# Performance work log

Measured on AMD Instinct MI355X. Metric: run time of the kernel, lower is better.

## Reference

```python
import jax, jax.numpy as jnp
import numpy as np

NUM_HEADS = 8


def setup_inputs() -> dict:
    key = jax.random.key(0)
    ks = jax.random.split(key, 8)
    B, N, H, W = 8, 1024, 32, 32
    dim = H * W  # 1024
    x1 = jax.random.normal(ks[0], (B, N, H, W), dtype=jnp.float32)
    x2 = jax.random.normal(ks[1], (B, N, H, W), dtype=jnp.float32)
    conv_w = jax.random.normal(ks[2], (N, 2 * N, 3, 3), dtype=jnp.float32) * 0.01
    conv_b = jnp.zeros((N,), dtype=jnp.float32)
    wq = jax.random.normal(ks[3], (dim, dim), dtype=jnp.float32) * 0.02
    wk = jax.random.normal(ks[4], (dim, dim), dtype=jnp.float32) * 0.02
    wv = jax.random.normal(ks[5], (dim, dim), dtype=jnp.float32) * 0.02
    proj_w = jax.random.normal(ks[6], (dim, dim), dtype=jnp.float32) * 0.02
    proj_b = jnp.zeros((dim,), dtype=jnp.float32)
    return {"x1": x1, "x2": x2, "conv_w": conv_w, "conv_b": conv_b,
            "wq": wq, "wk": wk, "wv": wv, "proj_w": proj_w, "proj_b": proj_b}


def reference(x1, x2, conv_w, conv_b, wq, wk, wv, proj_w, proj_b):
    B, N, H, W = x1.shape
    C = H * W
    nh = NUM_HEADS
    hd = C // nh
    scale = hd ** -0.5

    # conv_cat: Conv2d(2N -> N, k=3, pad=1) on channel-concatenated inputs
    x_cat = jnp.concatenate([x1, x2], axis=1)  # [B, 2N, H, W]
    x_cat = jax.lax.conv_general_dilated(
        x_cat, conv_w, window_strides=(1, 1), padding=((1, 1), (1, 1)),
        dimension_numbers=("NCHW", "OIHW", "NCHW"))
    x_cat = x_cat + conv_b[None, :, None, None]
    x_cat = x_cat.reshape(B, N, C)  # [B, N, C]

    # torch Linear: y = x @ W.T (no bias, qkv_bias=False)
    def heads(t):  # [B, N, C] -> [B, nh, N, hd]
        return t.reshape(B, N, nh, hd).transpose(0, 2, 1, 3)

    q = heads(x1.reshape(B, N, C) @ wq.T)
    k = heads(x_cat @ wk.T)
    v = heads(x_cat @ wv.T)

    # attention: softmax(q k^T * scale) v   (dropout is identity at p=0)
    attn = jnp.einsum("bhnd,bhmd->bhnm", q, k) * scale
    attn = jax.nn.softmax(attn, axis=-1)
    x_attn = jnp.einsum("bhnm,bhmd->bhnd", attn, v)  # [B, nh, N, hd]
    x_attn = x_attn.transpose(0, 2, 1, 3).reshape(B, N, C)

    out = (x_attn @ proj_w.T + proj_b).reshape(B, N, H, W) + x1
    return out
```

## Files before the change

### kernel.cpp

```cpp
#include <hip/hip_runtime.h>
#include <hip/hip_bf16.h>
#include <cstdint>
#include <cstddef>

typedef __attribute__((ext_vector_type(8))) short short8;
typedef __attribute__((ext_vector_type(4))) float f32x4;
typedef unsigned short u16;

static __device__ __forceinline__ u16 f2bf(float f) {
  __hip_bfloat16 h = __float2bfloat16(f);
  return *reinterpret_cast<u16*>(&h);
}

static __device__ __forceinline__ void gload16(const void* g, void* l) {
  __builtin_amdgcn_global_load_lds(
      (const __attribute__((address_space(1))) void*)g,
      (__attribute__((address_space(3))) void*)l, 16, 0, 0);
}


__global__ void cast4_k(const float* __restrict__ a, const float* __restrict__ b,
                        const float* __restrict__ c, const float* __restrict__ d,
                        u16* __restrict__ oa, u16* __restrict__ ob,
                        u16* __restrict__ oc, u16* __restrict__ od) {
  const int which = blockIdx.y;
  const float* src = (which == 0) ? a : (which == 1) ? b : (which == 2) ? c : d;
  u16* dst = (which == 0) ? oa : (which == 1) ? ob : (which == 2) ? oc : od;
  int i = blockIdx.x * 256 + threadIdx.x;
  float4 v = ((const float4*)src)[i];
  union { u16 u[4]; uint2 p; } r;
  r.u[0] = f2bf(v.x); r.u[1] = f2bf(v.y); r.u[2] = f2bf(v.z); r.u[3] = f2bf(v.w);
  ((uint2*)dst)[i] = r.p;
}

__global__ void build_int2(const float* __restrict__ x1, const float* __restrict__ x2,
                           u16* __restrict__ in_t, u16* __restrict__ x1b) {
  __shared__ float tile[64][65];
  const int it = blockIdx.x;
  const int st = blockIdx.y;
  const int b  = blockIdx.z;
  const int i0 = it * 64, s0 = st * 64;
  const bool isx1 = (i0 < 1024);
  const float* src = isx1
      ? x1 + ((size_t)b * 1024 + i0) * 1024
      : x2 + ((size_t)b * 1024 + (i0 - 1024)) * 1024;
  const int t = threadIdx.x;
  #pragma unroll
  for (int jj = 0; jj < 16; ++jj) {
    int idx = jj * 256 + t;
    int ii = idx >> 6, si = idx & 63;
    float v = src[(size_t)ii * 1024 + s0 + si];
    tile[ii][si] = v;
    if (isx1)
      x1b[((size_t)b * 1024 + i0 + ii) * 1024 + s0 + si] = f2bf(v);
  }
  __syncthreads();
  #pragma unroll
  for (int jj = 0; jj < 16; ++jj) {
    int idx = jj * 256 + t;
    int si = idx >> 6, ii = idx & 63;
    in_t[((size_t)b * 1024 + s0 + si) * 2048 + i0 + ii] = f2bf(tile[ii][si]);
  }
}

__global__ void pack_wp(const float* __restrict__ cw, u16* __restrict__ Wp) {
  __shared__ float sb[2304];
  const int blk = blockIdx.x;
  const int t = threadIdx.x;
  const size_t base = (size_t)blk * 2304;
  #pragma unroll
  for (int jj = 0; jj < 9; ++jj) sb[jj * 256 + t] = cw[base + jj * 256 + t];
  __syncthreads();
  const int p = blk * 256 + t;
  #pragma unroll
  for (int q = 0; q < 9; ++q)
    Wp[(size_t)q * 2097152 + p] = f2bf(sb[t * 9 + q]);
}

__global__ void zero_k(u16* z) { z[threadIdx.x] = 0; }

__global__ void addc_k(const float* __restrict__ p, const float* __restrict__ bias,
                       u16* __restrict__ xc) {
  __shared__ float tile[64][65];
  const int st = blockIdx.x;
  const int ot = blockIdx.y;
  const int b  = blockIdx.z;
  const int s0 = st * 64, o0 = ot * 64;
  const int t = threadIdx.x;
  const float* p1 = p + 8388608;
  #pragma unroll
  for (int jj = 0; jj < 16; ++jj) {
    int idx = jj * 256 + t;
    int si = idx >> 6, oi = idx & 63;
    const size_t m = ((size_t)b * 1024 + s0 + si) * 1024 + o0 + oi;
    tile[si][oi] = p[m] + p1[m] + bias[o0 + oi];
  }
  __syncthreads();
  #pragma unroll
  for (int jj = 0; jj < 16; ++jj) {
    int idx = jj * 256 + t;
    int oi = idx >> 6, si = idx & 63;
    xc[((size_t)b * 1024 + o0 + oi) * 1024 + s0 + si] = f2bf(tile[si][oi]);
  }
}

enum { GM_PLAIN = 0, GM_VT = 1, GM_PROJ = 2, GM_CONV = 3, GM_KV = 4 };

template<int MODE>
__global__ __launch_bounds__(512, 2)
void gemm3_k(const u16* __restrict__ A, const u16* __restrict__ B,
             u16* __restrict__ Cb, float* __restrict__ Cf,
             const float* __restrict__ bias, const float* __restrict__ resid,
             int Ktot, int ntn_sh) {
  __shared__ u16 lds[3 * 24576];
  const int tid = threadIdx.x;
  const int lane = tid & 63;
  const int w = tid >> 6;
  const int l15 = lane & 15, l4 = lane >> 4;

  const int nwg = gridDim.x;
  const int bid = blockIdx.x;
  const int lb = (bid & 7) * (nwg >> 3) + (bid >> 3);
  const int tm = lb >> ntn_sh;
  const int tn = lb & ((1 << ntn_sh) - 1);
  const int row0 = tm * 256, col0 = tn * 128;
  const int wr = (w >> 1) * 64, wc = (w & 1) * 64;

  const int sr = w * 8 + (lane >> 3);
  const int pp = (lane & 7) ^ (lane >> 3);

  f32x4 acc[4][4];
  #pragma unroll
  for (int i = 0; i < 4; ++i)
    #pragma unroll
    for (int jj = 0; jj < 4; ++jj)
      acc[i][jj] = (f32x4){0.f, 0.f, 0.f, 0.f};

  const int nK = Ktot >> 6;

  auto stage = [&](int kt, u16* buf) {
    u16* da = buf + (size_t)w * 512;
    u16* db = buf + 16384 + (size_t)w * 512;
    const int k0 = kt << 6;
    #pragma unroll
    for (int u = 0; u < 4; ++u) {
      const u16* ga = A + (size_t)(row0 + u * 64 + sr) * Ktot + k0 + pp * 8;
      gload16(ga, da + u * 4096);
    }
    #pragma unroll
    for (int u = 0; u < 2; ++u) {
      const u16* gb = B + (size_t)(col0 + u * 64 + sr) * Ktot + k0 + pp * 8;
      gload16(gb, db + u * 4096);
    }
  };

  auto compute = [&](const u16* buf) {
    const char* Ar = (const char*)buf;
    const char* Br = (const char*)(buf + 16384);
    #pragma unroll
    for (int ks = 0; ks < 2; ++ks) {
      const int bcol = ((ks << 6) + (l4 << 4)) ^ ((l15 & 7) << 4);
      short8 av[4], bv[4];
      #pragma unroll
      for (int mi = 0; mi < 4; ++mi)
        av[mi] = *(const short8*)(Ar + (wr + mi * 16 + l15) * 128 + bcol);
      #pragma unroll
      for (int ni = 0; ni < 4; ++ni)
        bv[ni] = *(const short8*)(Br + (wc + ni * 16 + l15) * 128 + bcol);
      __builtin_amdgcn_s_setprio(1);
      #pragma unroll
      for (int mi = 0; mi < 4; ++mi)
        #pragma unroll
        for (int ni = 0; ni < 4; ++ni)
          acc[mi][ni] = __builtin_amdgcn_mfma_f32_16x16x32_bf16(av[mi], bv[ni], acc[mi][ni], 0, 0, 0);
      __builtin_amdgcn_s_setprio(0);
    }
  };

  u16* pb0 = lds;
  u16* pb1 = lds + 24576;
  u16* pb2 = lds + 49152;

  stage(0, pb0);
  stage(1, pb1);
  for (int t = 0; t < nK; ++t) {
    if (t + 1 < nK) {
      asm volatile("s_waitcnt vmcnt(6)" ::: "memory");
    } else {
      asm volatile("s_waitcnt vmcnt(0)" ::: "memory");
    }
    __builtin_amdgcn_s_barrier();
    if (t + 2 < nK) stage(t + 2, pb2);
    compute(pb0);
    u16* tmp = pb0; pb0 = pb1; pb1 = pb2; pb2 = tmp;
  }

  #pragma unroll
  for (int mi = 0; mi < 4; ++mi) {
    #pragma unroll
    for (int ni = 0; ni < 4; ++ni) {
      #pragma unroll
      for (int j = 0; j < 4; ++j) {
        const int grow = row0 + wr + mi * 16 + l4 * 4 + j;
        const int gcol = col0 + wc + ni * 16 + l15;
        const float v = acc[mi][ni][j];
        if constexpr (MODE == GM_PLAIN) {
          Cb[((size_t)grow << 10) + gcol] = f2bf(v);
        } else if constexpr (MODE == GM_PROJ) {
          const size_t o = ((size_t)grow << 10) + gcol;
          Cf[o] = v + bias[gcol] + resid[o];
        }
      }
    }
  }
}

template<int MODE>
__global__ __launch_bounds__(512, 4)
void gemm5_k(const u16* __restrict__ A, const u16* __restrict__ B,
             u16* __restrict__ Cb, u16* __restrict__ Cb2,
             const u16* __restrict__ zb, int Ktot, int ntn_sh) {
  __shared__ u16 lds[3 * 12288];
  const int tid = threadIdx.x;
  const int lane = tid & 63;
  const int w = tid >> 6;
  const int l15 = lane & 15, l4 = lane >> 4;

  const int nwg = gridDim.x;
  const int bid = blockIdx.x;
  const int lb = (bid & 7) * (nwg >> 3) + (bid >> 3);
  const int tm = lb >> ntn_sh;
  const int tn = lb & ((1 << ntn_sh) - 1);
  const int row0 = tm * 256, col0 = tn * 128;
  const int wr = (w >> 1) * 64, wc = (w & 1) * 64;

  const int str = tid >> 2;
  const int sgc = tid & 3;

  f32x4 acc[4][4];
  #pragma unroll
  for (int i = 0; i < 4; ++i)
    #pragma unroll
    for (int jj = 0; jj < 4; ++jj)
      acc[i][jj] = (f32x4){0.f, 0.f, 0.f, 0.f};

  const int nKt = Ktot >> 5;

  auto stage = [&](int kt, u16* buf) {
    const int k0 = kt << 5;
    #pragma unroll
    for (int u = 0; u < 2; ++u) {
      const int r = u * 128 + str;
      const int swz = sgc ^ ((r >> 1) & 3);
      const u16* ga = A + (size_t)(row0 + r) * Ktot + k0 + swz * 8;
      gload16(ga, buf + ((size_t)u * 512 + tid) * 8);
    }
    {
      const int swz = sgc ^ ((str >> 1) & 3);
      const u16* gb = B + (size_t)(col0 + str) * Ktot + k0 + swz * 8;
      gload16(gb, buf + 8192 + (size_t)tid * 8);
    }
  };

  auto compute = [&](const u16* buf) {
    short8 av[4], bv[4];
    #pragma unroll
    for (int mi = 0; mi < 4; ++mi) {
      const int row = wr + mi * 16 + l15;
      const int g = l4 ^ ((row >> 1) & 3);
      av[mi] = *(const short8*)(buf + row * 32 + g * 8);
    }
    #pragma unroll
    for (int ni = 0; ni < 4; ++ni) {
      const int row = wc + ni * 16 + l15;
      const int g = l4 ^ ((row >> 1) & 3);
      bv[ni] = *(const short8*)(buf + 8192 + row * 32 + g * 8);
    }
    __builtin_amdgcn_s_setprio(1);
    #pragma unroll
    for (int mi = 0; mi < 4; ++mi)
      #pragma unroll
      for (int ni = 0; ni < 4; ++ni)
        acc[mi][ni] = __builtin_amdgcn_mfma_f32_16x16x32_bf16(av[mi], bv[ni], acc[mi][ni], 0, 0, 0);
    __builtin_amdgcn_s_setprio(0);
  };

  u16* pb0 = lds;
  u16* pb1 = lds + 12288;
  u16* pb2 = lds + 24576;

  stage(0, pb0);
  stage(1, pb1);
  for (int t = 0; t < nKt; ++t) {
    if (t + 1 < nKt) {
      asm volatile("s_waitcnt vmcnt(3)" ::: "memory");
    } else {
      asm volatile("s_waitcnt vmcnt(0)" ::: "memory");
    }
    __builtin_amdgcn_s_barrier();
    if (t + 2 < nKt) stage(t + 2, pb2);
    compute(pb0);
    u16* tmp = pb0; pb0 = pb1; pb1 = pb2; pb2 = tmp;
  }

  #pragma unroll
  for (int mi = 0; mi < 4; ++mi) {
    #pragma unroll
    for (int ni = 0; ni < 4; ++ni) {
      #pragma unroll
      for (int j = 0; j < 4; ++j) {
        const int grow = row0 + wr + mi * 16 + l4 * 4 + j;
        const int gcol = col0 + wc + ni * 16 + l15;
        const float v = acc[mi][ni][j];
        if constexpr (MODE == GM_KV) {
          if (gcol < 1024) {
            Cb[((size_t)grow << 10) + gcol] = f2bf(v);
          } else {
            const int c = gcol - 1024;
            const int b = grow >> 10, ms = grow & 1023;
            const int h = c >> 7, d = c & 127;
            Cb2[((size_t)((b * 8 + h) * 128 + d) << 10) + ms] = f2bf(v);
          }
        }
      }
    }
  }
}

template<int SPLITK>
__global__ __launch_bounds__(256, 2)
void gemm6_k(const u16* __restrict__ A, const u16* __restrict__ B,
             float* __restrict__ Cf, const u16* __restrict__ zb,
             int Ktot, int ntn_sh) {
  __shared__ u16 lds[3 * 12288];
  const int tid = threadIdx.x;
  const int lane = tid & 63;
  const int w = tid >> 6;
  const int l15 = lane & 15, l4 = lane >> 4;

  const int nwg = gridDim.x;
  const int bid = blockIdx.x;
  const int lb = (bid & 7) * (nwg >> 3) + (bid >> 3);
  int kz = 0, lbt = lb;
  if constexpr (SPLITK) { kz = lb >> 8; lbt = lb & 255; }
  const int tm = lbt >> ntn_sh;
  const int tn = lbt & ((1 << ntn_sh) - 1);
  const int row0 = tm * 256, col0 = tn * 128;
  const int wr = w * 64;

  const int str = tid >> 2;
  const int sgc = tid & 3;
  const int swz = sgc ^ ((str >> 1) & 3);

  int am[4], ay[4], ax[4];
  #pragma unroll
  for (int u = 0; u < 4; ++u) {
    const int m = row0 + u * 64 + str;
    am[u] = m;
    const int s = m & 1023;
    ay[u] = s >> 5; ax[u] = s & 31;
  }

  f32x4 acc[4][8];
  #pragma unroll
  for (int i = 0; i < 4; ++i)
    #pragma unroll
    for (int jj = 0; jj < 8; ++jj)
      acc[i][jj] = (f32x4){0.f, 0.f, 0.f, 0.f};

  const int nKt = Ktot >> 5;
  const int kbase = SPLITK ? kz * Ktot : 0;

  auto stage = [&](int kt, u16* buf) {
    const int gk0 = kbase + (kt << 5);
    const int q = gk0 >> 11;
    const int ks0 = gk0 & 2047;
    const int qd = (q >= 6) ? 2 : (q >= 3) ? 1 : 0;
    const int dy = qd - 1, dx = q - qd * 3 - 1;
    const int dd = (dy << 5) + dx;
    #pragma unroll
    for (int u = 0; u < 4; ++u) {
      const int yy = ay[u] + dy, xx = ax[u] + dx;
      const bool valid = ((unsigned)yy < 32u) && ((unsigned)xx < 32u);
      const u16* ga = valid ? A + (((size_t)(am[u] + dd)) << 11) + ks0 + swz * 8 : zb;
      gload16(ga, buf + ((size_t)u * 256 + tid) * 8);
    }
    #pragma unroll
    for (int u = 0; u < 2; ++u) {
      const u16* gb = B + ((size_t)q << 21) + ((size_t)(col0 + u * 64 + str) << 11) + ks0 + swz * 8;
      gload16(gb, buf + 8192 + ((size_t)u * 256 + tid) * 8);
    }
  };

  auto compute = [&](const u16* buf) {
    short8 av[4], bv[8];
    #pragma unroll
    for (int mi = 0; mi < 4; ++mi) {
      const int row = wr + mi * 16 + l15;
      const int g = l4 ^ ((row >> 1) & 3);
      av[mi] = *(const short8*)(buf + row * 32 + g * 8);
    }
    #pragma unroll
    for (int ni = 0; ni < 8; ++ni) {
      const int row = ni * 16 + l15;
      const int g = l4 ^ ((row >> 1) & 3);
      bv[ni] = *(const short8*)(buf + 8192 + row * 32 + g * 8);
    }
    __builtin_amdgcn_s_setprio(1);
    #pragma unroll
    for (int mi = 0; mi < 4; ++mi)
      #pragma unroll
      for (int ni = 0; ni < 8; ++ni)
        acc[mi][ni] = __builtin_amdgcn_mfma_f32_16x16x32_bf16(av[mi], bv[ni], acc[mi][ni], 0, 0, 0);
    __builtin_amdgcn_s_setprio(0);
  };

  u16* pb0 = lds;
  u16* pb1 = lds + 12288;
  u16* pb2 = lds + 24576;

  stage(0, pb0);
  stage(1, pb1);
  for (int t = 0; t < nKt; ++t) {
    if (t + 1 < nKt) {
      asm volatile("s_waitcnt vmcnt(6)" ::: "memory");
    } else {
      asm volatile("s_waitcnt vmcnt(0)" ::: "memory");
    }
    __builtin_amdgcn_s_barrier();
    if (t + 2 < nKt) stage(t + 2, pb2);
    compute(pb0);
    u16* tmp = pb0; pb0 = pb1; pb1 = pb2; pb2 = tmp;
  }

  #pragma unroll
  for (int mi = 0; mi < 4; ++mi) {
    #pragma unroll
    for (int ni = 0; ni < 8; ++ni) {
      #pragma unroll
      for (int j = 0; j < 4; ++j) {
        const int grow = row0 + wr + mi * 16 + l4 * 4 + j;
        const int gcol = col0 + ni * 16 + l15;
        Cf[(size_t)kz * 8388608 + ((size_t)grow << 10) + gcol] = acc[mi][ni][j];
      }
    }
  }
}

__global__ __launch_bounds__(256, 2)
void attn2_k(const u16* __restrict__ Q, const u16* __restrict__ K,
             const u16* __restrict__ Vt, u16* __restrict__ O) {
  __shared__ u16 Ks[2][64 * 128];
  __shared__ u16 Vs[2][128 * 64];
  __shared__ u16 Plds[4][16 * 80];
  const int mtile = blockIdx.x;
  const int bh = blockIdx.y;
  const int b = bh >> 3, h = bh & 7;
  const int tid = threadIdx.x, lane = tid & 63, w = tid >> 6;
  const int l15 = lane & 15, l4 = lane >> 4;

  short8 qf[4];
  {
    const int qrow = b * 1024 + mtile * 64 + w * 16 + l15;
    const u16* qb = Q + ((size_t)qrow << 10) + h * 128;
    #pragma unroll
    for (int kk = 0; kk < 4; ++kk)
      qf[kk] = *(const short8*)(qb + kk * 32 + l4 * 8);
  }

  f32x4 o[8];
  #pragma unroll
  for (int db = 0; db < 8; ++db) o[db] = (f32x4){0.f, 0.f, 0.f, 0.f};
  float mrow[4], lrow[4];
  #pragma unroll
  for (int j = 0; j < 4; ++j) { mrow[j] = -1e30f; lrow[j] = 0.f; }
  const float scale = 0.08838834764831845f;

  auto stageKV = [&](int kt, int half) {
    #pragma unroll
    for (int j = 0; j < 4; ++j) {
      const int c = (j * 4 + w) * 64 + lane;
      const int r = c >> 4;
      const int coff = (((c & 15) ^ (r & 7)) << 3);
      const u16* gp = K + ((size_t)(b * 1024 + kt * 64 + r) << 10) + h * 128 + coff;
      gload16(gp, (void*)(Ks[half] + (j * 4 + w) * 512));
    }
    #pragma unroll
    for (int j = 0; j < 4; ++j) {
      const int c = (j * 4 + w) * 64 + lane;
      const int r = c >> 3;
      const int coff = (((c & 7) ^ (r & 7)) << 3);
      const u16* gp = Vt + ((size_t)((b * 8 + h) * 128 + r) << 10) + kt * 64 + coff;
      gload16(gp, (void*)(Vs[half] + (j * 4 + w) * 512));
    }
  };

  stageKV(0, 0);
  for (int kt = 0; kt < 16; ++kt) {
    const int cur = kt & 1;
    asm volatile("s_waitcnt vmcnt(0)" ::: "memory");
    __builtin_amdgcn_s_barrier();
    if (kt + 1 < 16) stageKV(kt + 1, cur ^ 1);

    const u16* ks_ = Ks[cur];
    const u16* vs_ = Vs[cur];
    f32x4 s[4];
    #pragma unroll
    for (int cb = 0; cb < 4; ++cb) {
      s[cb] = (f32x4){0.f, 0.f, 0.f, 0.f};
      #pragma unroll
      for (int kk = 0; kk < 4; ++kk) {
        const int col = (kk * 32 + l4 * 8) ^ ((l15 & 7) << 3);
        short8 bK = *(const short8*)(ks_ + (cb * 16 + l15) * 128 + col);
        s[cb] = __builtin_amdgcn_mfma_f32_16x16x32_bf16(qf[kk], bK, s[cb], 0, 0, 0);
      }
    }
    #pragma unroll
    for (int cb = 0; cb < 4; ++cb) {
      s[cb][0] *= scale; s[cb][1] *= scale; s[cb][2] *= scale; s[cb][3] *= scale;
    }
    #pragma unroll
    for (int j = 0; j < 4; ++j) {
      float mx = fmaxf(fmaxf(s[0][j], s[1][j]), fmaxf(s[2][j], s[3][j]));
      #pragma unroll
      for (int off = 8; off >= 1; off >>= 1)
        mx = fmaxf(mx, __shfl_xor(mx, off, 64));
      const float mn = fmaxf(mrow[j], mx);
      const float fac = __expf(mrow[j] - mn);
      mrow[j] = mn;
      float rs = 0.f;
      #pragma unroll
      for (int cb = 0; cb < 4; ++cb) {
        const float p = __expf(s[cb][j] - mn);
        s[cb][j] = p;
        rs += p;
      }
      #pragma unroll
      for (int off = 8; off >= 1; off >>= 1)
        rs += __shfl_xor(rs, off, 64);
      lrow[j] = lrow[j] * fac + rs;
      #pragma unroll
      for (int db = 0; db < 8; ++db) o[db][j] *= fac;
    }
    u16* pl = Plds[w];
    #pragma unroll
    for (int cb = 0; cb < 4; ++cb)
      #pragma unroll
      for (int j = 0; j < 4; ++j)
        pl[(l4 * 4 + j) * 80 + cb * 16 + l15] = f2bf(s[cb][j]);
    asm volatile("s_waitcnt lgkmcnt(0)" ::: "memory");
    __builtin_amdgcn_sched_barrier(0);
    short8 ap[2];
    #pragma unroll
    for (int ks2 = 0; ks2 < 2; ++ks2)
      ap[ks2] = *(const short8*)(pl + l15 * 80 + ks2 * 32 + l4 * 8);
    #pragma unroll
    for (int db = 0; db < 8; ++db) {
      #pragma unroll
      for (int ks2 = 0; ks2 < 2; ++ks2) {
        const int col = (ks2 * 32 + l4 * 8) ^ ((l15 & 7) << 3);
        short8 bV = *(const short8*)(vs_ + (db * 16 + l15) * 64 + col);
        o[db] = __builtin_amdgcn_mfma_f32_16x16x32_bf16(ap[ks2], bV, o[db], 0, 0, 0);
      }
    }
  }
  #pragma unroll
  for (int db = 0; db < 8; ++db) {
    #pragma unroll
    for (int j = 0; j < 4; ++j) {
      const int grow = b * 1024 + mtile * 64 + w * 16 + l4 * 4 + j;
      const int gcol = h * 128 + db * 16 + l15;
      O[((size_t)grow << 10) + gcol] = f2bf(o[db][j] / lrow[j]);
    }
  }
}


extern "C" void kernel_launch(void* const* d_in, const int* in_sizes, int n_in,
                              void* d_out, int out_size, void* d_ws, size_t ws_size,
                              hipStream_t stream) {
  const float* x1     = (const float*)d_in[0];
  const float* x2     = (const float*)d_in[1];
  const float* conv_w = (const float*)d_in[2];
  const float* conv_b = (const float*)d_in[3];
  const float* wq     = (const float*)d_in[4];
  const float* wk     = (const float*)d_in[5];
  const float* wv     = (const float*)d_in[6];
  const float* proj_w = (const float*)d_in[7];
  const float* proj_b = (const float*)d_in[8];
  float* out = (float*)d_out;

  char* ws = (char*)d_ws;
  size_t off = 0;
  auto alloc = [&](size_t bytes) -> void* {
    void* p = ws + off;
    off += (bytes + 255) & ~(size_t)255;
    return p;
  };
  u16* x1b  = (u16*)alloc(8192ULL * 1024 * 2);
  u16* in_t = (u16*)alloc(8ULL * 1024 * 2048 * 2);
  u16* Wp   = (u16*)alloc(9ULL * 2097152 * 2);
  u16* wqb  = (u16*)alloc(1048576ULL * 2);
  u16* wkb  = (u16*)alloc(1048576ULL * 2);
  u16* wvb  = (u16*)alloc(1048576ULL * 2);
  u16* pjb  = (u16*)alloc(1048576ULL * 2);
  u16* xc   = (u16*)alloc(8192ULL * 1024 * 2);
  u16* Qb   = (u16*)alloc(8192ULL * 1024 * 2);
  u16* Kb   = (u16*)alloc(8192ULL * 1024 * 2);
  u16* Vtb  = (u16*)alloc(8192ULL * 1024 * 2);
  u16* Ob   = (u16*)alloc(8192ULL * 1024 * 2);
  u16* zb   = (u16*)alloc(256);
  float* pConv = (float*)Qb;

  cast4_k<<<dim3(1024, 4), 256, 0, stream>>>(wq, wk, wv, proj_w, wqb, wkb, wvb, pjb);
  build_int2<<<dim3(32, 16, 8), 256, 0, stream>>>(x1, x2, in_t, x1b);
  pack_wp<<<8192, 256, 0, stream>>>(conv_w, Wp);
  zero_k<<<1, 128, 0, stream>>>(zb);

  gemm6_k<1><<<512, 256, 0, stream>>>(in_t, Wp, pConv, zb, 9216, 3);
  addc_k<<<dim3(16, 16, 8), 256, 0, stream>>>(pConv, conv_b, xc);
  gemm3_k<GM_PLAIN><<<256, 512, 0, stream>>>(x1b, wqb, Qb, nullptr, nullptr, nullptr, 1024, 3);
  gemm5_k<GM_KV><<<512, 512, 0, stream>>>(xc, wkb, Kb, Vtb, zb, 1024, 4);
  attn2_k<<<dim3(16, 64), 256, 0, stream>>>(Qb, Kb, Vtb, Ob);
  gemm3_k<GM_PROJ><<<256, 512, 0, stream>>>(Ob, pjb, nullptr, out, proj_b, x1, 1024, 3);
}
```

Baseline: 573.7 us.

## Replace implicit-GEMM conv with padded-halo conv kernel reusing staged input across taps

The input transpose now writes into a zero-padded 34x34 spatial layout, cleared first with a memset, so the conv needs no bounds checks or zero-buffer redirects. A new conv kernel stages a halo tile of input rows (8 image rows plus borders) per 32-channel chunk once, and reuses it across all nine filter taps by offsetting LDS row indices, streaming only the per-tap weight tiles. This cuts repeated global loads of the shifted input, 9x per channel chunk in the old version, at the cost of a memset over the padded buffer and more complex vmcnt/barrier scheduling.

```diff
diff --git a/kernel.cpp b/kernel.cpp
--- a/kernel.cpp
+++ b/kernel.cpp
@@ -33,8 +33,8 @@
   ((uint2*)dst)[i] = r.p;
 }
 
-__global__ void build_int2(const float* __restrict__ x1, const float* __restrict__ x2,
-                           u16* __restrict__ in_t, u16* __restrict__ x1b) {
+__global__ void build_pad(const float* __restrict__ x1, const float* __restrict__ x2,
+                          u16* __restrict__ in_t_pad, u16* __restrict__ x1b) {
   __shared__ float tile[64][65];
   const int it = blockIdx.x;
   const int st = blockIdx.y;
@@ -59,7 +59,9 @@
   for (int jj = 0; jj < 16; ++jj) {
     int idx = jj * 256 + t;
     int si = idx >> 6, ii = idx & 63;
-    in_t[((size_t)b * 1024 + s0 + si) * 2048 + i0 + ii] = f2bf(tile[ii][si]);
+    const int s = s0 + si;
+    const int prow = (b * 34 + (s >> 5) + 1) * 34 + (s & 31) + 1;
+    in_t_pad[(size_t)prow * 2048 + i0 + ii] = f2bf(tile[ii][si]);
   }
 }
 
@@ -76,8 +78,6 @@
   for (int q = 0; q < 9; ++q)
     Wp[(size_t)q * 2097152 + p] = f2bf(sb[t * 9 + q]);
 }
-
-__global__ void zero_k(u16* z) { z[threadIdx.x] = 0; }
 
 __global__ void addc_k(const float* __restrict__ p, const float* __restrict__ bias,
                        u16* __restrict__ xc) {
@@ -104,7 +104,139 @@
   }
 }
 
-enum { GM_PLAIN = 0, GM_VT = 1, GM_PROJ = 2, GM_CONV = 3, GM_KV = 4 };
+enum { GM_PLAIN = 0, GM_PROJ = 2, GM_KV = 4 };
+
+__global__ __launch_bounds__(256, 2)
+void conv7_k(const u16* __restrict__ Ap, const u16* __restrict__ B,
+             float* __restrict__ Cf) {
+  __shared__ u16 lds[2 * 12288 + 3 * 4096];
+  const int tid = threadIdx.x;
+  const int lane = tid & 63, w = tid >> 6;
+  const int l15 = lane & 15, l4 = lane >> 4;
+
+  const int bid = blockIdx.x;
+  const int lb = (bid & 7) * 64 + (bid >> 3);
+  const int kz = lb >> 8;
+  const int tile = lb & 255;
+  const int tm = tile >> 3, tn = tile & 7;
+  const int row0 = tm * 256, col0 = tn * 128;
+  const int b = tm >> 2;
+  const int y0 = (tm & 3) * 8;
+  const int hb = (b * 34 + y0) * 34;
+  const int wr = w * 64;
+  const int chbase = kz * 1024;
+
+  int pr[4];
+  #pragma unroll
+  for (int mi = 0; mi < 4; ++mi) {
+    const int m = row0 + wr + mi * 16 + l15;
+    const int y = (m >> 5) & 31, x = m & 31;
+    pr[mi] = (y - y0 + 1) * 34 + x + 1;
+  }
+
+  const int srow = tid >> 2;
+  const int sgc = tid & 3;
+
+  f32x4 acc[4][8];
+  #pragma unroll
+  for (int i = 0; i < 4; ++i)
+    #pragma unroll
+    for (int jj = 0; jj < 8; ++jj)
+      acc[i][jj] = (f32x4){0.f, 0.f, 0.f, 0.f};
+
+  auto stageHalo = [&](int cc, int half) {
+    u16* dst = lds + half * 12288;
+    #pragma unroll
+    for (int rnd = 0; rnd < 6; ++rnd) {
+      const int row = rnd * 64 + srow;
+      const int g = sgc ^ ((row >> 1) & 3);
+      const u16* src = Ap + (size_t)(hb + row) * 2048 + chbase + cc * 32 + g * 8;
+      gload16(src, dst + (size_t)(rnd * 256 + tid) * 8);
+    }
+  };
+  auto stageB = [&](int cc, int q) {
+    u16* dst = lds + 24576 + (q % 3) * 4096;
+    #pragma unroll
+    for (int rnd = 0; rnd < 2; ++rnd) {
+      const int r = rnd * 64 + srow;
+      const int g = sgc ^ ((r >> 1) & 3);
+      const u16* src = B + ((size_t)q << 21) + (size_t)(col0 + r) * 2048
+                       + chbase + cc * 32 + g * 8;
+      gload16(src, dst + (size_t)(rnd * 256 + tid) * 8);
+    }
+  };
+
+  constexpr int ddt[9] = {-35, -34, -33, -1, 0, 1, 33, 34, 35};
+  constexpr int NC = 32;
+
+  stageHalo(0, 0);
+  stageHalo(1, 1);
+  stageB(0, 0);
+  stageB(0, 1);
+
+  for (int cc = 0; cc < NC; ++cc) {
+    const u16* hcur = lds + (cc & 1) * 12288;
+    const bool interior = (cc >= 1 && cc <= NC - 2);
+    #pragma unroll
+    for (int q = 0; q < 9; ++q) {
+      if ((q == 1 || q == 2) && interior) {
+        asm volatile("s_waitcnt vmcnt(8)" ::: "memory");
+      } else if (q == 8 && cc == NC - 1) {
+        asm volatile("s_waitcnt vmcnt(0)" ::: "memory");
+      } else {
+        asm volatile("s_waitcnt vmcnt(2)" ::: "memory");
+      }
+      __builtin_amdgcn_s_barrier();
+      {
+        const int gp2 = cc * 9 + q + 2;
+        if (gp2 <= NC * 9 - 1) {
+          int qS = q + 2, ccS = cc;
+          if (qS >= 9) { qS -= 9; ccS += 1; }
+          stageB(ccS, qS);
+        }
+        if (q == 0 && cc >= 1 && cc <= NC - 2)
+          stageHalo(cc + 1, (cc + 1) & 1);
+      }
+      {
+        const u16* bq = lds + 24576 + (q % 3) * 4096;
+        const int dd = ddt[q];
+        short8 av[4], bv[8];
+        #pragma unroll
+        for (int mi = 0; mi < 4; ++mi) {
+          const int hr = pr[mi] + dd;
+          const int g = l4 ^ ((hr >> 1) & 3);
+          av[mi] = *(const short8*)(hcur + hr * 32 + g * 8);
+        }
+        #pragma unroll
+        for (int ni = 0; ni < 8; ++ni) {
+          const int r = ni * 16 + l15;
+          const int g = l4 ^ ((r >> 1) & 3);
+          bv[ni] = *(const short8*)(bq + r * 32 + g * 8);
+        }
+        __builtin_amdgcn_s_setprio(1);
+        #pragma unroll
+        for (int mi = 0; mi < 4; ++mi)
+          #pragma unroll
+          for (int ni = 0; ni < 8; ++ni)
+            acc[mi][ni] = __builtin_amdgcn_mfma_f32_16x16x32_bf16(av[mi], bv[ni], acc[mi][ni], 0, 0, 0);
+        __builtin_amdgcn_s_setprio(0);
+      }
+    }
+  }
+
+  #pragma unroll
+  for (int mi = 0; mi < 4; ++mi) {
+    #pragma unroll
+    for (int ni = 0; ni < 8; ++ni) {
+      #pragma unroll
+      for (int j = 0; j < 4; ++j) {
+        const int grow = row0 + wr + mi * 16 + l4 * 4 + j;
+        const int gcol = col0 + ni * 16 + l15;
+        Cf[(size_t)kz * 8388608 + ((size_t)grow << 10) + gcol] = acc[mi][ni][j];
+      }
+    }
+  }
+}
 
 template<int MODE>
 __global__ __launch_bounds__(512, 2)
@@ -219,7 +351,7 @@
 __global__ __launch_bounds__(512, 4)
 void gemm5_k(const u16* __restrict__ A, const u16* __restrict__ B,
              u16* __restrict__ Cb, u16* __restrict__ Cb2,
-             const u16* __restrict__ zb, int Ktot, int ntn_sh) {
+             int Ktot, int ntn_sh) {
   __shared__ u16 lds[3 * 12288];
   const int tid = threadIdx.x;
   const int lane = tid & 63;
@@ -327,126 +459,6 @@
   }
 }
 
-template<int SPLITK>
-__global__ __launch_bounds__(256, 2)
-void gemm6_k(const u16* __restrict__ A, const u16* __restrict__ B,
-             float* __restrict__ Cf, const u16* __restrict__ zb,
-             int Ktot, int ntn_sh) {
-  __shared__ u16 lds[3 * 12288];
-  const int tid = threadIdx.x;
-  const int lane = tid & 63;
-  const int w = tid >> 6;
-  const int l15 = lane & 15, l4 = lane >> 4;
-
-  const int nwg = gridDim.x;
-  const int bid = blockIdx.x;
-  const int lb = (bid & 7) * (nwg >> 3) + (bid >> 3);
-  int kz = 0, lbt = lb;
-  if constexpr (SPLITK) { kz = lb >> 8; lbt = lb & 255; }
-  const int tm = lbt >> ntn_sh;
-  const int tn = lbt & ((1 << ntn_sh) - 1);
-  const int row0 = tm * 256, col0 = tn * 128;
-  const int wr = w * 64;
-
-  const int str = tid >> 2;
-  const int sgc = tid & 3;
-  const int swz = sgc ^ ((str >> 1) & 3);
-
-  int am[4], ay[4], ax[4];
-  #pragma unroll
-  for (int u = 0; u < 4; ++u) {
-    const int m = row0 + u * 64 + str;
-    am[u] = m;
-    const int s = m & 1023;
-    ay[u] = s >> 5; ax[u] = s & 31;
-  }
-
-  f32x4 acc[4][8];
-  #pragma unroll
-  for (int i = 0; i < 4; ++i)
-    #pragma unroll
-    for (int jj = 0; jj < 8; ++jj)
-      acc[i][jj] = (f32x4){0.f, 0.f, 0.f, 0.f};
-
-  const int nKt = Ktot >> 5;
-  const int kbase = SPLITK ? kz * Ktot : 0;
-
-  auto stage = [&](int kt, u16* buf) {
-    const int gk0 = kbase + (kt << 5);
-    const int q = gk0 >> 11;
-    const int ks0 = gk0 & 2047;
-    const int qd = (q >= 6) ? 2 : (q >= 3) ? 1 : 0;
-    const int dy = qd - 1, dx = q - qd * 3 - 1;
-    const int dd = (dy << 5) + dx;
-    #pragma unroll
-    for (int u = 0; u < 4; ++u) {
-      const int yy = ay[u] + dy, xx = ax[u] + dx;
-      const bool valid = ((unsigned)yy < 32u) && ((unsigned)xx < 32u);
-      const u16* ga = valid ? A + (((size_t)(am[u] + dd)) << 11) + ks0 + swz * 8 : zb;
-      gload16(ga, buf + ((size_t)u * 256 + tid) * 8);
-    }
-    #pragma unroll
-    for (int u = 0; u < 2; ++u) {
-      const u16* gb = B + ((size_t)q << 21) + ((size_t)(col0 + u * 64 + str) << 11) + ks0 + swz * 8;
-      gload16(gb, buf + 8192 + ((size_t)u * 256 + tid) * 8);
-    }
-  };
-
-  auto compute = [&](const u16* buf) {
-    short8 av[4], bv[8];
-    #pragma unroll
-    for (int mi = 0; mi < 4; ++mi) {
-      const int row = wr + mi * 16 + l15;
-      const int g = l4 ^ ((row >> 1) & 3);
-      av[mi] = *(const short8*)(buf + row * 32 + g * 8);
-    }
-    #pragma unroll
-    for (int ni = 0; ni < 8; ++ni) {
-      const int row = ni * 16 + l15;
-      const int g = l4 ^ ((row >> 1) & 3);
-      bv[ni] = *(const short8*)(buf + 8192 + row * 32 + g * 8);
-    }
-    __builtin_amdgcn_s_setprio(1);
-    #pragma unroll
-    for (int mi = 0; mi < 4; ++mi)
-      #pragma unroll
-      for (int ni = 0; ni < 8; ++ni)
-        acc[mi][ni] = __builtin_amdgcn_mfma_f32_16x16x32_bf16(av[mi], bv[ni], acc[mi][ni], 0, 0, 0);
-    __builtin_amdgcn_s_setprio(0);
-  };
-
-  u16* pb0 = lds;
-  u16* pb1 = lds + 12288;
-  u16* pb2 = lds + 24576;
-
-  stage(0, pb0);
-  stage(1, pb1);
-  for (int t = 0; t < nKt; ++t) {
-    if (t + 1 < nKt) {
-      asm volatile("s_waitcnt vmcnt(6)" ::: "memory");
-    } else {
-      asm volatile("s_waitcnt vmcnt(0)" ::: "memory");
-    }
-    __builtin_amdgcn_s_barrier();
-    if (t + 2 < nKt) stage(t + 2, pb2);
-    compute(pb0);
-    u16* tmp = pb0; pb0 = pb1; pb1 = pb2; pb2 = tmp;
-  }
-
-  #pragma unroll
-  for (int mi = 0; mi < 4; ++mi) {
-    #pragma unroll
-    for (int ni = 0; ni < 8; ++ni) {
-      #pragma unroll
-      for (int j = 0; j < 4; ++j) {
-        const int grow = row0 + wr + mi * 16 + l4 * 4 + j;
-        const int gcol = col0 + ni * 16 + l15;
-        Cf[(size_t)kz * 8388608 + ((size_t)grow << 10) + gcol] = acc[mi][ni][j];
-      }
-    }
-  }
-}
-
 __global__ __launch_bounds__(256, 2)
 void attn2_k(const u16* __restrict__ Q, const u16* __restrict__ K,
              const u16* __restrict__ Vt, u16* __restrict__ O) {
@@ -598,7 +610,8 @@
     return p;
   };
   u16* x1b  = (u16*)alloc(8192ULL * 1024 * 2);
-  u16* in_t = (u16*)alloc(8ULL * 1024 * 2048 * 2);
+  u16* in_t_pad = (u16*)alloc((9248ULL + 96) * 2048 * 2);
+  const size_t pad_bytes = 9248ULL * 2048 * 2;
   u16* Wp   = (u16*)alloc(9ULL * 2097152 * 2);
   u16* wqb  = (u16*)alloc(1048576ULL * 2);
   u16* wkb  = (u16*)alloc(1048576ULL * 2);
@@ -609,18 +622,17 @@
   u16* Kb   = (u16*)alloc(8192ULL * 1024 * 2);
   u16* Vtb  = (u16*)alloc(8192ULL * 1024 * 2);
   u16* Ob   = (u16*)alloc(8192ULL * 1024 * 2);
-  u16* zb   = (u16*)alloc(256);
   float* pConv = (float*)Qb;
 
+  (void)hipMemsetAsync(in_t_pad, 0, pad_bytes + 96ULL * 2048 * 2, stream);
   cast4_k<<<dim3(1024, 4), 256, 0, stream>>>(wq, wk, wv, proj_w, wqb, wkb, wvb, pjb);
-  build_int2<<<dim3(32, 16, 8), 256, 0, stream>>>(x1, x2, in_t, x1b);
+  build_pad<<<dim3(32, 16, 8), 256, 0, stream>>>(x1, x2, in_t_pad, x1b);
   pack_wp<<<8192, 256, 0, stream>>>(conv_w, Wp);
-  zero_k<<<1, 128, 0, stream>>>(zb);
-
-  gemm6_k<1><<<512, 256, 0, stream>>>(in_t, Wp, pConv, zb, 9216, 3);
+
+  conv7_k<<<512, 256, 0, stream>>>(in_t_pad, Wp, pConv);
   addc_k<<<dim3(16, 16, 8), 256, 0, stream>>>(pConv, conv_b, xc);
   gemm3_k<GM_PLAIN><<<256, 512, 0, stream>>>(x1b, wqb, Qb, nullptr, nullptr, nullptr, 1024, 3);
-  gemm5_k<GM_KV><<<512, 512, 0, stream>>>(xc, wkb, Kb, Vtb, zb, 1024, 4);
+  gemm5_k<GM_KV><<<512, 512, 0, stream>>>(xc, wkb, Kb, Vtb, 1024, 4);
   attn2_k<<<dim3(16, 64), 256, 0, stream>>>(Qb, Kb, Vtb, Ob);
   gemm3_k<GM_PROJ><<<256, 512, 0, stream>>>(Ob, pjb, nullptr, out, proj_b, x1, 1024, 3);
 }
```

Measured after the change: 564.3 us. No clear change (-1.6%).
